# Kernel optimization log

Hardware: AMD Instinct MI355X
Metric: run time of the kernel (lower is better)

Reference implementation:

```python
import jax, jax.numpy as jnp
import numpy as np

N_NODES = 100000
N_EDGES = 1600000
N_GRAPHS = 2048
DIM_IN, DIM_H, DIM_FC, DIM_OUT = 128, 128, 256, 8


def _glorot(key, shape):
    fan_in, fan_out = shape[0], shape[1]
    lim = float(np.sqrt(6.0 / (fan_in + fan_out)))
    return jax.random.uniform(key, shape, jnp.float32, -lim, lim)


def setup_inputs() -> dict:
    key = jax.random.key(0)
    ks = jax.random.split(key, 16)
    x = jax.random.normal(ks[0], (N_NODES, DIM_IN), jnp.float32)
    edge_index = jax.random.randint(ks[1], (2, N_EDGES), 0, N_NODES, jnp.int64)
    batch = jnp.sort(jax.random.randint(ks[2], (N_NODES,), 0, N_GRAPHS, jnp.int64))
    inp = {"x": x, "edge_index": edge_index, "batch": batch}
    # GraphConv layers: W_rel [in,out], W_root [in,out], b [out]
    dims = [(DIM_IN, DIM_H), (DIM_H, DIM_H), (DIM_H, DIM_H), (DIM_H, DIM_H)]
    for i, (di, do) in enumerate(dims, start=1):
        inp[f"W{i}_rel"] = _glorot(ks[2 + 3 * i], (di, do))
        inp[f"W{i}_root"] = _glorot(ks[3 + 3 * i], (di, do))
        inp[f"b{i}"] = jnp.zeros((do,), jnp.float32)
    inp["fc_w"] = _glorot(ks[3], (DIM_H, DIM_FC))
    inp["fc_b"] = jnp.zeros((DIM_FC,), jnp.float32)
    inp["reg_w"] = _glorot(ks[4], (DIM_FC, DIM_OUT))
    inp["reg_b"] = jnp.zeros((DIM_OUT,), jnp.float32)
    return inp


def _graph_conv(x, src, dst, w_rel, w_root, b):
    # PyG GraphConv (aggr='add'): out_i = W_rel @ sum_{j->i} x_j + W_root @ x_i + b
    agg = jax.ops.segment_sum(x[src], dst, num_segments=N_NODES)  # [N, d_in]
    return agg @ w_rel + x @ w_root + b


def reference(x, edge_index, batch,
              W1_rel, W1_root, b1, W2_rel, W2_root, b2,
              W3_rel, W3_root, b3, W4_rel, W4_root, b4,
              fc_w, fc_b, reg_w, reg_b):
    src, dst = edge_index[0], edge_index[1]
    h = jax.nn.relu(_graph_conv(x, src, dst, W1_rel, W1_root, b1))
    h = jax.nn.relu(_graph_conv(h, src, dst, W2_rel, W2_root, b2))
    h = jax.nn.relu(_graph_conv(h, src, dst, W3_rel, W3_root, b3))
    h = jax.nn.relu(_graph_conv(h, src, dst, W4_rel, W4_root, b4))
    # global_mean_pool over graphs
    sums = jax.ops.segment_sum(h, batch, num_segments=N_GRAPHS)  # [G, d]
    cnt = jax.ops.segment_sum(jnp.ones((h.shape[0],), h.dtype), batch,
                              num_segments=N_GRAPHS)
    pooled = sums / jnp.maximum(cnt, 1.0)[:, None]
    # dropout is identity at inference
    hfc = pooled @ fc_w + fc_b
    return hfc @ reg_w + reg_b  # [G, dim_out]
```

## Files before the change

### kernel.cpp

```cpp
#include <hip/hip_runtime.h>

#define N_NODES 100000
#define N_EDGES 1600000
#define N_GRAPHS 2048
#define DIM 128

#define NBUK 196
#define BUKSH 9
#define NCH 256
#define EPB 6250
#define NMAT (NBUK * NCH)

typedef short short8v __attribute__((ext_vector_type(8)));
typedef float float4v __attribute__((ext_vector_type(4)));

__device__ __forceinline__ unsigned short f2bf(float f) {
  union { float f; unsigned u; } x; x.f = f;
  unsigned r = x.u + 0x7fffu + ((x.u >> 16) & 1u);
  return (unsigned short)(r >> 16);
}
__device__ __forceinline__ float bfhi2f(unsigned bits) {
  union { unsigned u; float f; } x; x.u = bits; return x.f;
}
__device__ __forceinline__ void accum8(float* p, uint4 v) {
  p[0] += bfhi2f(v.x << 16); p[1] += bfhi2f(v.x & 0xffff0000u);
  p[2] += bfhi2f(v.y << 16); p[3] += bfhi2f(v.y & 0xffff0000u);
  p[4] += bfhi2f(v.z << 16); p[5] += bfhi2f(v.z & 0xffff0000u);
  p[6] += bfhi2f(v.w << 16); p[7] += bfhi2f(v.w & 0xffff0000u);
}

__global__ __launch_bounds__(256) void k_bcount(const int* __restrict__ dst, int* __restrict__ cntmat) {
  __shared__ int cnt[NBUK];
  int b = blockIdx.x, t = threadIdx.x;
  if (t < NBUK) cnt[t] = 0;
  __syncthreads();
  int e0 = b * EPB;
  for (int j = t; j < EPB; j += 256) atomicAdd(&cnt[dst[e0 + j] >> BUKSH], 1);
  __syncthreads();
  if (t < NBUK) cntmat[t * NCH + b] = cnt[t];
}

__global__ __launch_bounds__(256) void k_scan1g(const int* __restrict__ in, int n,
                                                int* __restrict__ tmp, int* __restrict__ bsum) {
  __shared__ int sh[256];
  int b = blockIdx.x, t = threadIdx.x;
  int base = b * 1024 + t * 4;
  int v[4], s = 0;
#pragma unroll
  for (int i = 0; i < 4; i++) { v[i] = (base + i < n) ? in[base + i] : 0; s += v[i]; }
  sh[t] = s;
  __syncthreads();
  for (int off = 1; off < 256; off <<= 1) {
    int x = (t >= off) ? sh[t - off] : 0;
    __syncthreads();
    sh[t] += x;
    __syncthreads();
  }
  int run = sh[t] - s;
#pragma unroll
  for (int i = 0; i < 4; i++) { run += v[i]; if (base + i < n) tmp[base + i] = run; }
  if (t == 255) bsum[b] = sh[255];
}

__global__ void k_scan2g(int* __restrict__ bsum, int nb) {
  __shared__ int sh[128];
  int t = threadIdx.x;
  int v = (t < nb) ? bsum[t] : 0;
  sh[t] = v;
  __syncthreads();
  for (int off = 1; off < 128; off <<= 1) {
    int x = (t >= off) ? sh[t - off] : 0;
    __syncthreads();
    sh[t] += x;
    __syncthreads();
  }
  if (t < nb) bsum[t] = sh[t] - v;
}

__global__ __launch_bounds__(256) void k_exc(const int* __restrict__ tmp, const int* __restrict__ bsum,
                                             const int* __restrict__ in, int n, int* __restrict__ outExc) {
  int i = blockIdx.x * 256 + threadIdx.x;
  if (i < n) outExc[i] = tmp[i] + bsum[i >> 10] - in[i];
}

__global__ __launch_bounds__(256) void k_bscatter(const int* __restrict__ src, const int* __restrict__ dst,
                                                  const int* __restrict__ base, int2* __restrict__ epk) {
  __shared__ int cur[NBUK];
  int b = blockIdx.x, t = threadIdx.x;
  if (t < NBUK) cur[t] = base[t * NCH + b];
  __syncthreads();
  int e0 = b * EPB;
  for (int j = t; j < EPB; j += 256) {
    int s = src[e0 + j], d = dst[e0 + j];
    int pos = atomicAdd(&cur[d >> BUKSH], 1);
    epk[pos] = make_int2(s, d);
  }
}

__global__ __launch_bounds__(256) void k_bfinish(const int2* __restrict__ epk, const int* __restrict__ base,
                                                 int* __restrict__ rowptr, int* __restrict__ col) {
  __shared__ int a[512];
  __shared__ int sh[256];
  int k = blockIdx.x, t = threadIdx.x;
  int bstart = base[k * NCH];
  int bend = (k + 1 < NBUK) ? base[(k + 1) * NCH] : N_EDGES;
  a[t] = 0; a[t + 256] = 0;
  __syncthreads();
  for (int i = bstart + t; i < bend; i += 256) atomicAdd(&a[epk[i].y - (k << BUKSH)], 1);
  __syncthreads();
  int c0 = a[2 * t], c1 = a[2 * t + 1];
  int s = c0 + c1;
  sh[t] = s;
  __syncthreads();
  for (int off = 1; off < 256; off <<= 1) {
    int x = (t >= off) ? sh[t - off] : 0;
    __syncthreads();
    sh[t] += x;
    __syncthreads();
  }
  int excl = sh[t] - s;
  int st0 = bstart + excl;
  int st1 = st0 + c0;
  int g0 = (k << BUKSH) + 2 * t, g1 = g0 + 1;
  if (g0 < N_NODES) rowptr[g0] = st0;
  if (g1 < N_NODES) rowptr[g1] = st1;
  if (k == NBUK - 1 && t == 0) rowptr[N_NODES] = N_EDGES;
  __syncthreads();
  a[2 * t] = st0; a[2 * t + 1] = st1;
  __syncthreads();
  for (int i = bstart + t; i < bend; i += 256) {
    int2 e = epk[i];
    int pos = atomicAdd(&a[e.y - (k << BUKSH)], 1);
    col[pos] = e.x;
  }
}

__global__ __launch_bounds__(256) void k_gptr(const int* __restrict__ batch, int* __restrict__ gptr) {
  int i = blockIdx.x * 256 + threadIdx.x;
  if (i >= N_NODES) return;
  int b = batch[i];
  int a = (i == 0) ? -1 : batch[i - 1];
  for (int g = a + 1; g <= b; g++) gptr[g] = i;
  if (i == N_NODES - 1) {
    for (int g = b + 1; g <= N_GRAPHS; g++) gptr[g] = N_NODES;
  }
}

__global__ __launch_bounds__(256) void k_cvtx(const float* __restrict__ x, unsigned short* __restrict__ h) {
  int i = blockIdx.x * 256 + threadIdx.x;
  if (i < N_NODES * DIM / 4) {
    float4 v = ((const float4*)x)[i];
    unsigned lo = (unsigned)f2bf(v.x) | ((unsigned)f2bf(v.y) << 16);
    unsigned hi = (unsigned)f2bf(v.z) | ((unsigned)f2bf(v.w) << 16);
    ((uint2*)h)[i] = make_uint2(lo, hi);
  }
}

__global__ __launch_bounds__(256) void k_cvtw(const float* w0, const float* w1, const float* w2, const float* w3,
                                              const float* w4, const float* w5, const float* w6, const float* w7,
                                              unsigned short* __restrict__ wbF) {
  int i = blockIdx.x * 256 + threadIdx.x;
  if (i < 4 * 8 * 8 * 64 * 8) {
    int j = i & 7, l = (i >> 3) & 63, c = (i >> 9) & 7, kc = (i >> 12) & 7, layer = i >> 15;
    int m = layer * 2 + (kc >> 2);
    const float* w;
    switch (m) {
      case 0: w = w0; break; case 1: w = w1; break; case 2: w = w2; break; case 3: w = w3; break;
      case 4: w = w4; break; case 5: w = w5; break; case 6: w = w6; break; default: w = w7; break;
    }
    int kin = (kc & 3) * 32 + ((l >> 4) * 8) + j;
    int n = c * 16 + (l & 15);
    wbF[i] = f2bf(w[kin * 128 + n]);
  }
}

__global__ __launch_bounds__(256, 8) void k_fused(const int* __restrict__ rowptr,
                                                  const int* __restrict__ col,
                                                  const unsigned short* __restrict__ hIn,
                                                  const unsigned short* __restrict__ wbF,
                                                  const float* __restrict__ bias,
                                                  unsigned short* __restrict__ hOut) {
  __shared__ uint4 As[1024];
  const int t = threadIdx.x;
  const int wave = t >> 6, lane = t & 63;
  const int wrow0 = blockIdx.x * 64 + wave * 16;
  const int sub = lane >> 4, li = lane & 15;

  for (int ri = 0; ri < 16; ri += 2) {
    int nodeA = wrow0 + ri;
    int nodeB = nodeA + 1;
    float pA[8], pB[8];
#pragma unroll
    for (int j = 0; j < 8; j++) { pA[j] = 0.f; pB[j] = 0.f; }
    int aS1 = 0, bS1 = 0, eA = 0, eB = 0;
    if (nodeA < N_NODES) { eA = rowptr[nodeA]; aS1 = rowptr[nodeA + 1]; }
    if (nodeB < N_NODES) { eB = rowptr[nodeB]; bS1 = rowptr[nodeB + 1]; }

    while (eA + 8 <= aS1 && eB + 8 <= bS1) {
      int cA0 = col[eA + sub], cA1 = col[eA + 4 + sub];
      int cB0 = col[eB + sub], cB1 = col[eB + 4 + sub];
      uint4 vA0 = *(const uint4*)(hIn + (size_t)cA0 * DIM + li * 8);
      uint4 vA1 = *(const uint4*)(hIn + (size_t)cA1 * DIM + li * 8);
      uint4 vB0 = *(const uint4*)(hIn + (size_t)cB0 * DIM + li * 8);
      uint4 vB1 = *(const uint4*)(hIn + (size_t)cB1 * DIM + li * 8);
      accum8(pA, vA0);
      accum8(pA, vA1);
      accum8(pB, vB0);
      accum8(pB, vB1);
      eA += 8; eB += 8;
    }
    for (; eA + 16 <= aS1; eA += 16) {
      int c0 = col[eA + sub], c1 = col[eA + 4 + sub], c2 = col[eA + 8 + sub], c3 = col[eA + 12 + sub];
      uint4 v0 = *(const uint4*)(hIn + (size_t)c0 * DIM + li * 8);
      uint4 v1 = *(const uint4*)(hIn + (size_t)c1 * DIM + li * 8);
      uint4 v2 = *(const uint4*)(hIn + (size_t)c2 * DIM + li * 8);
      uint4 v3 = *(const uint4*)(hIn + (size_t)c3 * DIM + li * 8);
      accum8(pA, v0); accum8(pA, v1); accum8(pA, v2); accum8(pA, v3);
    }
    if (eA + 8 <= aS1) {
      int c0 = col[eA + sub], c1 = col[eA + 4 + sub];
      uint4 v0 = *(const uint4*)(hIn + (size_t)c0 * DIM + li * 8);
      uint4 v1 = *(const uint4*)(hIn + (size_t)c1 * DIM + li * 8);
      accum8(pA, v0); accum8(pA, v1);
      eA += 8;
    }
    if (eA + 4 <= aS1) {
      int c0 = col[eA + sub];
      uint4 v0 = *(const uint4*)(hIn + (size_t)c0 * DIM + li * 8);
      accum8(pA, v0);
      eA += 4;
    }
    if (eA + sub < aS1) {
      int c0 = col[eA + sub];
      uint4 v0 = *(const uint4*)(hIn + (size_t)c0 * DIM + li * 8);
      accum8(pA, v0);
    }
    for (; eB + 16 <= bS1; eB += 16) {
      int c0 = col[eB + sub], c1 = col[eB + 4 + sub], c2 = col[eB + 8 + sub], c3 = col[eB + 12 + sub];
      uint4 v0 = *(const uint4*)(hIn + (size_t)c0 * DIM + li * 8);
      uint4 v1 = *(const uint4*)(hIn + (size_t)c1 * DIM + li * 8);
      uint4 v2 = *(const uint4*)(hIn + (size_t)c2 * DIM + li * 8);
      uint4 v3 = *(const uint4*)(hIn + (size_t)c3 * DIM + li * 8);
      accum8(pB, v0); accum8(pB, v1); accum8(pB, v2); accum8(pB, v3);
    }
    if (eB + 8 <= bS1) {
      int c0 = col[eB + sub], c1 = col[eB + 4 + sub];
      uint4 v0 = *(const uint4*)(hIn + (size_t)c0 * DIM + li * 8);
      uint4 v1 = *(const uint4*)(hIn + (size_t)c1 * DIM + li * 8);
      accum8(pB, v0); accum8(pB, v1);
      eB += 8;
    }
    if (eB + 4 <= bS1) {
      int c0 = col[eB + sub];
      uint4 v0 = *(const uint4*)(hIn + (size_t)c0 * DIM + li * 8);
      accum8(pB, v0);
      eB += 4;
    }
    if (eB + sub < bS1) {
      int c0 = col[eB + sub];
      uint4 v0 = *(const uint4*)(hIn + (size_t)c0 * DIM + li * 8);
      accum8(pB, v0);
    }

#pragma unroll
    for (int j = 0; j < 8; j++) {
      pA[j] += __shfl_xor(pA[j], 16, 64);
      pA[j] += __shfl_xor(pA[j], 32, 64);
      pB[j] += __shfl_xor(pB[j], 16, 64);
      pB[j] += __shfl_xor(pB[j], 32, 64);
    }
    if (sub == 0) {
      uint4 oA, oB;
      oA.x = (unsigned)f2bf(pA[0]) | ((unsigned)f2bf(pA[1]) << 16);
      oA.y = (unsigned)f2bf(pA[2]) | ((unsigned)f2bf(pA[3]) << 16);
      oA.z = (unsigned)f2bf(pA[4]) | ((unsigned)f2bf(pA[5]) << 16);
      oA.w = (unsigned)f2bf(pA[6]) | ((unsigned)f2bf(pA[7]) << 16);
      oB.x = (unsigned)f2bf(pB[0]) | ((unsigned)f2bf(pB[1]) << 16);
      oB.y = (unsigned)f2bf(pB[2]) | ((unsigned)f2bf(pB[3]) << 16);
      oB.z = (unsigned)f2bf(pB[4]) | ((unsigned)f2bf(pB[5]) << 16);
      oB.w = (unsigned)f2bf(pB[6]) | ((unsigned)f2bf(pB[7]) << 16);
      As[(wave * 16 + li) * 16 + (ri ^ li)] = oA;
      As[(wave * 16 + li) * 16 + ((ri + 1) ^ li)] = oB;
    }
  }

  float4v acc[8];
#pragma unroll
  for (int c2 = 0; c2 < 8; c2++)
#pragma unroll
    for (int i = 0; i < 4; i++) acc[c2][i] = 0.f;

#pragma unroll
  for (int kc = 0; kc < 4; kc++) {
    int c = kc * 4 + sub;
    short8v afr = *(const short8v*)&As[(wave * 16 + c) * 16 + (li ^ c)];
#pragma unroll
    for (int c2 = 0; c2 < 8; c2++) {
      short8v bfr = *(const short8v*)(wbF + (size_t)((kc * 8 + c2) * 64 + lane) * 8);
      acc[c2] = __builtin_amdgcn_mfma_f32_16x16x32_bf16(afr, bfr, acc[c2], 0, 0, 0);
    }
  }

#pragma unroll
  for (int j = 0; j < 4; j++) {
    int idx = j * 64 + lane;
    int r = idx >> 4, c = idx & 15;
    int rsrc = wrow0 + r; if (rsrc > N_NODES - 1) rsrc = N_NODES - 1;
    uint4 v = *(const uint4*)(hIn + (size_t)rsrc * DIM + c * 8);
    As[(wave * 16 + c) * 16 + (r ^ c)] = v;
  }

#pragma unroll
  for (int kc = 0; kc < 4; kc++) {
    int c = kc * 4 + sub;
    short8v afr = *(const short8v*)&As[(wave * 16 + c) * 16 + (li ^ c)];
#pragma unroll
    for (int c2 = 0; c2 < 8; c2++) {
      short8v bfr = *(const short8v*)(wbF + (size_t)(((4 + kc) * 8 + c2) * 64 + lane) * 8);
      acc[c2] = __builtin_amdgcn_mfma_f32_16x16x32_bf16(afr, bfr, acc[c2], 0, 0, 0);
    }
  }

  int rbase = wrow0 + sub * 4;
#pragma unroll
  for (int c2 = 0; c2 < 8; c2++) {
    int colidx = c2 * 16 + li;
    float bv = bias[colidx];
#pragma unroll
    for (int i = 0; i < 4; i++) {
      int row = rbase + i;
      if (row < N_NODES) {
        float v = acc[c2][i] + bv;
        v = v > 0.f ? v : 0.f;
        hOut[row * DIM + colidx] = f2bf(v);
      }
    }
  }
}

__global__ __launch_bounds__(256) void k_pool(const unsigned short* __restrict__ h,
                                              const int* __restrict__ gptr,
                                              float* __restrict__ pooledMean) {
  int g = blockIdx.x * 4 + (threadIdx.x >> 6);
  if (g >= N_GRAPHS) return;
  int lane = threadIdx.x & 63;
  int li = lane & 15;
  int s0 = gptr[g], s1 = gptr[g + 1];
  float p[8];
#pragma unroll
  for (int j = 0; j < 8; j++) p[j] = 0.f;
  int f1 = s1 * 16;
  for (int f = s0 * 16 + lane; f < f1; f += 64) {
    uint4 v = ((const uint4*)h)[f];
    accum8(p, v);
  }
#pragma unroll
  for (int j = 0; j < 8; j++) {
    p[j] += __shfl_xor(p[j], 16, 64);
    p[j] += __shfl_xor(p[j], 32, 64);
  }
  float inv = (s1 > s0) ? 1.f / (float)(s1 - s0) : 0.f;
  if (lane < 16) {
    float4 o0 = make_float4(p[0] * inv, p[1] * inv, p[2] * inv, p[3] * inv);
    float4 o1 = make_float4(p[4] * inv, p[5] * inv, p[6] * inv, p[7] * inv);
    *(float4*)(pooledMean + g * DIM + li * 8) = o0;
    *(float4*)(pooledMean + g * DIM + li * 8 + 4) = o1;
  }
}

__global__ __launch_bounds__(256) void k_fc(const float* __restrict__ pooledMean,
                                            const float* __restrict__ fc_w, const float* __restrict__ fc_b,
                                            const float* __restrict__ reg_w, const float* __restrict__ reg_b,
                                            float* __restrict__ out) {
  __shared__ float sp[128];
  __shared__ float shfc[256];
  __shared__ float red[64];
  int g = blockIdx.x, t = threadIdx.x;
  if (t < 128) sp[t] = pooledMean[g * DIM + t];
  __syncthreads();
  float a = fc_b[t];
  for (int k = 0; k < 128; k++) a += sp[k] * fc_w[k * 256 + t];
  shfc[t] = a;
  __syncthreads();
  if (t < 64) {
    int o = t & 7, seg = t >> 3;
    float r = 0.f;
    for (int j = seg * 32; j < seg * 32 + 32; j++) r += shfc[j] * reg_w[j * 8 + o];
    red[t] = r;
  }
  __syncthreads();
  if (t < 8) {
    float r = reg_b[t];
    for (int s = 0; s < 8; s++) r += red[s * 8 + t];
    out[g * 8 + t] = r;
  }
}

extern "C" void kernel_launch(void* const* d_in, const int* in_sizes, int n_in,
                              void* d_out, int out_size, void* d_ws, size_t ws_size,
                              hipStream_t stream) {
  (void)in_sizes; (void)n_in; (void)out_size; (void)ws_size;
  const float* x = (const float*)d_in[0];
  const int* ei = (const int*)d_in[1];
  const int* src = ei;
  const int* dst = ei + N_EDGES;
  const int* batch = (const int*)d_in[2];
  const float* Wrel[4]  = {(const float*)d_in[3], (const float*)d_in[6], (const float*)d_in[9],  (const float*)d_in[12]};
  const float* Wroot[4] = {(const float*)d_in[4], (const float*)d_in[7], (const float*)d_in[10], (const float*)d_in[13]};
  const float* bias[4]  = {(const float*)d_in[5], (const float*)d_in[8], (const float*)d_in[11], (const float*)d_in[14]};
  const float* fc_w  = (const float*)d_in[15];
  const float* fc_b  = (const float*)d_in[16];
  const float* reg_w = (const float*)d_in[17];
  const float* reg_b = (const float*)d_in[18];
  float* out = (float*)d_out;

  char* ws = (char*)d_ws;
  size_t off = 0;
  auto alloc = [&](size_t b) -> char* {
    char* p = ws + off;
    off = (off + b + 255) & ~(size_t)255;
    return p;
  };
  int* rowptr = (int*)alloc((N_NODES + 1) * 4);
  int* cntmat = (int*)alloc((size_t)NMAT * 4);
  int* tmpB   = (int*)alloc((size_t)NMAT * 4);
  int* bsumB  = (int*)alloc(128 * 4);
  int* base   = (int*)alloc((size_t)NMAT * 4);
  int2* epk   = (int2*)alloc((size_t)N_EDGES * 8);
  int* colws  = (int*)alloc((size_t)N_EDGES * 4);
  int* gptr   = (int*)alloc((N_GRAPHS + 1) * 4);
  unsigned short* wbF = (unsigned short*)alloc((size_t)4 * 32768 * 2);
  unsigned short* h_a = (unsigned short*)alloc((size_t)N_NODES * DIM * 2);
  unsigned short* h_b = (unsigned short*)alloc((size_t)N_NODES * DIM * 2);
  float* pooled = (float*)alloc((size_t)N_GRAPHS * DIM * 4);

  k_bcount<<<NCH, 256, 0, stream>>>(dst, cntmat);
  k_scan1g<<<NMAT / 1024, 256, 0, stream>>>(cntmat, NMAT, tmpB, bsumB);
  k_scan2g<<<1, 128, 0, stream>>>(bsumB, NMAT / 1024);
  k_exc<<<(NMAT + 255) / 256, 256, 0, stream>>>(tmpB, bsumB, cntmat, NMAT, base);
  k_bscatter<<<NCH, 256, 0, stream>>>(src, dst, base, epk);
  k_bfinish<<<NBUK, 256, 0, stream>>>(epk, base, rowptr, colws);

  k_gptr<<<(N_NODES + 255) / 256, 256, 0, stream>>>(batch, gptr);
  k_cvtx<<<(N_NODES * DIM / 4 + 255) / 256, 256, 0, stream>>>(x, h_a);
  k_cvtw<<<(4 * 32768 + 255) / 256, 256, 0, stream>>>(
      Wrel[0], Wroot[0], Wrel[1], Wroot[1], Wrel[2], Wroot[2], Wrel[3], Wroot[3], wbF);

  unsigned short* h_in = h_a;
  unsigned short* h_out = h_b;
  const int FB = (N_NODES + 63) / 64;
  for (int l = 0; l < 4; l++) {
    k_fused<<<FB, 256, 0, stream>>>(rowptr, colws, h_in, wbF + (size_t)l * 32768, bias[l], h_out);
    unsigned short* t2 = h_in; h_in = h_out; h_out = t2;
  }

  k_pool<<<(N_GRAPHS + 3) / 4, 256, 0, stream>>>(h_in, gptr, pooled);
  k_fc<<<N_GRAPHS, 256, 0, stream>>>(pooled, fc_w, fc_b, reg_w, reg_b, out);
}
```

Before: 506.3 us.

## Build CSR with two-pass radix sort so neighbour lists come out sorted by source

The CSR build becomes a two-pass bucket sort. Edges are first bucketed by source, then stably re-bucketed by destination, so each node's neighbour list is ordered by source index. Edge records are packed into 32-bit words instead of int2, which halves the scatter traffic. The aim is better cache locality for the row gathers in the four fused layers, at the cost of extra count, scan and scatter kernels in preprocessing.

Result: slower. 535.6 us (+5.8%).

```diff
diff --git a/kernel.cpp b/kernel.cpp
--- a/kernel.cpp
+++ b/kernel.cpp
@@ -10,6 +10,7 @@
 #define NCH 256
 #define EPB 6250
 #define NMAT (NBUK * NCH)
+#define NMATD (NBUK * NBUK)
 
 typedef short short8v __attribute__((ext_vector_type(8)));
 typedef float float4v __attribute__((ext_vector_type(4)));
@@ -29,13 +30,14 @@
   p[6] += bfhi2f(v.w << 16); p[7] += bfhi2f(v.w & 0xffff0000u);
 }
 
-__global__ __launch_bounds__(256) void k_bcount(const int* __restrict__ dst, int* __restrict__ cntmat) {
+
+__global__ __launch_bounds__(256) void k_bcount(const int* __restrict__ key, int* __restrict__ cntmat) {
   __shared__ int cnt[NBUK];
   int b = blockIdx.x, t = threadIdx.x;
   if (t < NBUK) cnt[t] = 0;
   __syncthreads();
   int e0 = b * EPB;
-  for (int j = t; j < EPB; j += 256) atomicAdd(&cnt[dst[e0 + j] >> BUKSH], 1);
+  for (int j = t; j < EPB; j += 256) atomicAdd(&cnt[key[e0 + j] >> BUKSH], 1);
   __syncthreads();
   if (t < NBUK) cntmat[t * NCH + b] = cnt[t];
 }
@@ -83,30 +85,67 @@
   if (i < n) outExc[i] = tmp[i] + bsum[i >> 10] - in[i];
 }
 
-__global__ __launch_bounds__(256) void k_bscatter(const int* __restrict__ src, const int* __restrict__ dst,
-                                                  const int* __restrict__ base, int2* __restrict__ epk) {
+__global__ __launch_bounds__(256) void k_bscatterS(const int* __restrict__ src, const int* __restrict__ dst,
+                                                   const int* __restrict__ baseS, unsigned* __restrict__ epkS) {
   __shared__ int cur[NBUK];
   int b = blockIdx.x, t = threadIdx.x;
-  if (t < NBUK) cur[t] = base[t * NCH + b];
+  if (t < NBUK) cur[t] = baseS[t * NCH + b];
   __syncthreads();
   int e0 = b * EPB;
   for (int j = t; j < EPB; j += 256) {
     int s = src[e0 + j], d = dst[e0 + j];
+    int pos = atomicAdd(&cur[s >> BUKSH], 1);
+    epkS[pos] = ((unsigned)(s & 511) << 17) | (unsigned)d;
+  }
+}
+
+__global__ __launch_bounds__(256) void k_bcountD(const unsigned* __restrict__ epkS,
+                                                 const int* __restrict__ baseS,
+                                                 int* __restrict__ cntmatD) {
+  __shared__ int cnt[NBUK];
+  int b = blockIdx.x, t = threadIdx.x;
+  if (t < NBUK) cnt[t] = 0;
+  __syncthreads();
+  int bstart = baseS[b * NCH];
+  int bend = (b + 1 < NBUK) ? baseS[(b + 1) * NCH] : N_EDGES;
+  for (int i = bstart + t; i < bend; i += 256) {
+    int d = epkS[i] & 0x1FFFF;
+    atomicAdd(&cnt[d >> BUKSH], 1);
+  }
+  __syncthreads();
+  if (t < NBUK) cntmatD[t * NBUK + b] = cnt[t];
+}
+
+__global__ __launch_bounds__(256) void k_bscatterD(const unsigned* __restrict__ epkS,
+                                                   const int* __restrict__ baseS,
+                                                   const int* __restrict__ baseD,
+                                                   unsigned* __restrict__ epkD) {
+  __shared__ int cur[NBUK];
+  int b = blockIdx.x, t = threadIdx.x;
+  if (t < NBUK) cur[t] = baseD[t * NBUK + b];
+  __syncthreads();
+  int bstart = baseS[b * NCH];
+  int bend = (b + 1 < NBUK) ? baseS[(b + 1) * NCH] : N_EDGES;
+  for (int i = bstart + t; i < bend; i += 256) {
+    unsigned pk = epkS[i];
+    int d = pk & 0x1FFFF;
+    int s = (b << BUKSH) | (int)(pk >> 17);
     int pos = atomicAdd(&cur[d >> BUKSH], 1);
-    epk[pos] = make_int2(s, d);
-  }
-}
-
-__global__ __launch_bounds__(256) void k_bfinish(const int2* __restrict__ epk, const int* __restrict__ base,
-                                                 int* __restrict__ rowptr, int* __restrict__ col) {
+    epkD[pos] = ((unsigned)(d & 511) << 17) | (unsigned)s;
+  }
+}
+
+__global__ __launch_bounds__(256) void k_bfinishD(const unsigned* __restrict__ epkD,
+                                                  const int* __restrict__ baseD,
+                                                  int* __restrict__ rowptr, int* __restrict__ col) {
   __shared__ int a[512];
   __shared__ int sh[256];
   int k = blockIdx.x, t = threadIdx.x;
-  int bstart = base[k * NCH];
-  int bend = (k + 1 < NBUK) ? base[(k + 1) * NCH] : N_EDGES;
+  int bstart = baseD[k * NBUK];
+  int bend = (k + 1 < NBUK) ? baseD[(k + 1) * NBUK] : N_EDGES;
   a[t] = 0; a[t + 256] = 0;
   __syncthreads();
-  for (int i = bstart + t; i < bend; i += 256) atomicAdd(&a[epk[i].y - (k << BUKSH)], 1);
+  for (int i = bstart + t; i < bend; i += 256) atomicAdd(&a[epkD[i] >> 17], 1);
   __syncthreads();
   int c0 = a[2 * t], c1 = a[2 * t + 1];
   int s = c0 + c1;
@@ -129,9 +168,9 @@
   a[2 * t] = st0; a[2 * t + 1] = st1;
   __syncthreads();
   for (int i = bstart + t; i < bend; i += 256) {
-    int2 e = epk[i];
-    int pos = atomicAdd(&a[e.y - (k << BUKSH)], 1);
-    col[pos] = e.x;
+    unsigned pk = epkD[i];
+    int pos = atomicAdd(&a[pk >> 17], 1);
+    col[pos] = (int)(pk & 0x1FFFF);
   }
 }
 
@@ -421,25 +460,34 @@
     off = (off + b + 255) & ~(size_t)255;
     return p;
   };
-  int* rowptr = (int*)alloc((N_NODES + 1) * 4);
-  int* cntmat = (int*)alloc((size_t)NMAT * 4);
-  int* tmpB   = (int*)alloc((size_t)NMAT * 4);
-  int* bsumB  = (int*)alloc(128 * 4);
-  int* base   = (int*)alloc((size_t)NMAT * 4);
-  int2* epk   = (int2*)alloc((size_t)N_EDGES * 8);
-  int* colws  = (int*)alloc((size_t)N_EDGES * 4);
-  int* gptr   = (int*)alloc((N_GRAPHS + 1) * 4);
+  int* rowptr  = (int*)alloc((N_NODES + 1) * 4);
+  int* cntmat  = (int*)alloc((size_t)NMAT * 4);
+  int* tmpB    = (int*)alloc((size_t)NMAT * 4);
+  int* bsumB   = (int*)alloc(128 * 4);
+  int* baseS   = (int*)alloc((size_t)NMAT * 4);
+  int* cntmatD = (int*)alloc((size_t)NMATD * 4);
+  int* baseD   = (int*)alloc((size_t)NMATD * 4);
+  unsigned* epkS = (unsigned*)alloc((size_t)N_EDGES * 4);
+  unsigned* epkD = (unsigned*)alloc((size_t)N_EDGES * 4);
+  int* colws   = (int*)alloc((size_t)N_EDGES * 4);
+  int* gptr    = (int*)alloc((N_GRAPHS + 1) * 4);
   unsigned short* wbF = (unsigned short*)alloc((size_t)4 * 32768 * 2);
   unsigned short* h_a = (unsigned short*)alloc((size_t)N_NODES * DIM * 2);
   unsigned short* h_b = (unsigned short*)alloc((size_t)N_NODES * DIM * 2);
   float* pooled = (float*)alloc((size_t)N_GRAPHS * DIM * 4);
 
-  k_bcount<<<NCH, 256, 0, stream>>>(dst, cntmat);
+  k_bcount<<<NCH, 256, 0, stream>>>(src, cntmat);
   k_scan1g<<<NMAT / 1024, 256, 0, stream>>>(cntmat, NMAT, tmpB, bsumB);
   k_scan2g<<<1, 128, 0, stream>>>(bsumB, NMAT / 1024);
-  k_exc<<<(NMAT + 255) / 256, 256, 0, stream>>>(tmpB, bsumB, cntmat, NMAT, base);
-  k_bscatter<<<NCH, 256, 0, stream>>>(src, dst, base, epk);
-  k_bfinish<<<NBUK, 256, 0, stream>>>(epk, base, rowptr, colws);
+  k_exc<<<(NMAT + 255) / 256, 256, 0, stream>>>(tmpB, bsumB, cntmat, NMAT, baseS);
+  k_bscatterS<<<NCH, 256, 0, stream>>>(src, dst, baseS, epkS);
+
+  k_bcountD<<<NBUK, 256, 0, stream>>>(epkS, baseS, cntmatD);
+  k_scan1g<<<(NMATD + 1023) / 1024, 256, 0, stream>>>(cntmatD, NMATD, tmpB, bsumB);
+  k_scan2g<<<1, 128, 0, stream>>>(bsumB, (NMATD + 1023) / 1024);
+  k_exc<<<(NMATD + 255) / 256, 256, 0, stream>>>(tmpB, bsumB, cntmatD, NMATD, baseD);
+  k_bscatterD<<<NBUK, 256, 0, stream>>>(epkS, baseS, baseD, epkD);
+  k_bfinishD<<<NBUK, 256, 0, stream>>>(epkD, baseD, rowptr, colws);
 
   k_gptr<<<(N_NODES + 255) / 256, 256, 0, stream>>>(batch, gptr);
   k_cvtx<<<(N_NODES * DIM / 4 + 255) / 256, 256, 0, stream>>>(x, h_a);
```

## Replace bucketed CSR build with direct global-atomic degree count and scatter

Applied to the files above, without the earlier changes.

Replaces the two-level bucketed counting sort for building the CSR with a direct per-node degree count using global atomics, a scan over node degrees, and a scatter of source indices via per-node atomic cursors. This removes the intermediate packed edge buffer and the bucket-finish pass, cutting memory traffic and kernel count. In exchange it relies on many global atomics and yields a non-deterministic neighbor order within each row. The final FC kernel is also restructured to process 16 graphs per block, reusing each fc_w load across graphs.

New measurement: 664.9 us. 31.3% more time.

```diff
diff --git a/kernel.cpp b/kernel.cpp
--- a/kernel.cpp
+++ b/kernel.cpp
@@ -4,12 +4,6 @@
 #define N_EDGES 1600000
 #define N_GRAPHS 2048
 #define DIM 128
-
-#define NBUK 196
-#define BUKSH 9
-#define NCH 256
-#define EPB 6250
-#define NMAT (NBUK * NCH)
 
 typedef short short8v __attribute__((ext_vector_type(8)));
 typedef float float4v __attribute__((ext_vector_type(4)));
@@ -29,15 +23,15 @@
   p[6] += bfhi2f(v.w << 16); p[7] += bfhi2f(v.w & 0xffff0000u);
 }
 
-__global__ __launch_bounds__(256) void k_bcount(const int* __restrict__ dst, int* __restrict__ cntmat) {
-  __shared__ int cnt[NBUK];
-  int b = blockIdx.x, t = threadIdx.x;
-  if (t < NBUK) cnt[t] = 0;
-  __syncthreads();
-  int e0 = b * EPB;
-  for (int j = t; j < EPB; j += 256) atomicAdd(&cnt[dst[e0 + j] >> BUKSH], 1);
-  __syncthreads();
-  if (t < NBUK) cntmat[t * NCH + b] = cnt[t];
+
+__global__ __launch_bounds__(256) void k_zero(int* __restrict__ p, int n) {
+  int i = blockIdx.x * 256 + threadIdx.x;
+  if (i < n) p[i] = 0;
+}
+
+__global__ __launch_bounds__(256) void k_dcnt(const int* __restrict__ dst, int* __restrict__ deg) {
+  int e = blockIdx.x * 256 + threadIdx.x;
+  if (e < N_EDGES) atomicAdd(&deg[dst[e]], 1);
 }
 
 __global__ __launch_bounds__(256) void k_scan1g(const int* __restrict__ in, int n,
@@ -77,61 +71,24 @@
   if (t < nb) bsum[t] = sh[t] - v;
 }
 
-__global__ __launch_bounds__(256) void k_exc(const int* __restrict__ tmp, const int* __restrict__ bsum,
-                                             const int* __restrict__ in, int n, int* __restrict__ outExc) {
+__global__ __launch_bounds__(256) void k_excR(const int* __restrict__ tmp, const int* __restrict__ bsum,
+                                              const int* __restrict__ deg, int n,
+                                              int* __restrict__ rowptr, int* __restrict__ cur) {
   int i = blockIdx.x * 256 + threadIdx.x;
-  if (i < n) outExc[i] = tmp[i] + bsum[i >> 10] - in[i];
-}
-
-__global__ __launch_bounds__(256) void k_bscatter(const int* __restrict__ src, const int* __restrict__ dst,
-                                                  const int* __restrict__ base, int2* __restrict__ epk) {
-  __shared__ int cur[NBUK];
-  int b = blockIdx.x, t = threadIdx.x;
-  if (t < NBUK) cur[t] = base[t * NCH + b];
-  __syncthreads();
-  int e0 = b * EPB;
-  for (int j = t; j < EPB; j += 256) {
-    int s = src[e0 + j], d = dst[e0 + j];
-    int pos = atomicAdd(&cur[d >> BUKSH], 1);
-    epk[pos] = make_int2(s, d);
-  }
-}
-
-__global__ __launch_bounds__(256) void k_bfinish(const int2* __restrict__ epk, const int* __restrict__ base,
-                                                 int* __restrict__ rowptr, int* __restrict__ col) {
-  __shared__ int a[512];
-  __shared__ int sh[256];
-  int k = blockIdx.x, t = threadIdx.x;
-  int bstart = base[k * NCH];
-  int bend = (k + 1 < NBUK) ? base[(k + 1) * NCH] : N_EDGES;
-  a[t] = 0; a[t + 256] = 0;
-  __syncthreads();
-  for (int i = bstart + t; i < bend; i += 256) atomicAdd(&a[epk[i].y - (k << BUKSH)], 1);
-  __syncthreads();
-  int c0 = a[2 * t], c1 = a[2 * t + 1];
-  int s = c0 + c1;
-  sh[t] = s;
-  __syncthreads();
-  for (int off = 1; off < 256; off <<= 1) {
-    int x = (t >= off) ? sh[t - off] : 0;
-    __syncthreads();
-    sh[t] += x;
-    __syncthreads();
-  }
-  int excl = sh[t] - s;
-  int st0 = bstart + excl;
-  int st1 = st0 + c0;
-  int g0 = (k << BUKSH) + 2 * t, g1 = g0 + 1;
-  if (g0 < N_NODES) rowptr[g0] = st0;
-  if (g1 < N_NODES) rowptr[g1] = st1;
-  if (k == NBUK - 1 && t == 0) rowptr[N_NODES] = N_EDGES;
-  __syncthreads();
-  a[2 * t] = st0; a[2 * t + 1] = st1;
-  __syncthreads();
-  for (int i = bstart + t; i < bend; i += 256) {
-    int2 e = epk[i];
-    int pos = atomicAdd(&a[e.y - (k << BUKSH)], 1);
-    col[pos] = e.x;
+  if (i < n) {
+    int ex = tmp[i] + bsum[i >> 10] - deg[i];
+    rowptr[i] = ex;
+    cur[i] = ex;
+    if (i == n - 1) rowptr[n] = ex + deg[i];
+  }
+}
+
+__global__ __launch_bounds__(256) void k_escatter(const int* __restrict__ src, const int* __restrict__ dst,
+                                                  int* __restrict__ cur, int* __restrict__ col) {
+  int e = blockIdx.x * 256 + threadIdx.x;
+  if (e < N_EDGES) {
+    int pos = atomicAdd(&cur[dst[e]], 1);
+    col[pos] = src[e];
   }
 }
 
@@ -368,31 +325,33 @@
   }
 }
 
-__global__ __launch_bounds__(256) void k_fc(const float* __restrict__ pooledMean,
-                                            const float* __restrict__ fc_w, const float* __restrict__ fc_b,
-                                            const float* __restrict__ reg_w, const float* __restrict__ reg_b,
-                                            float* __restrict__ out) {
-  __shared__ float sp[128];
-  __shared__ float shfc[256];
-  __shared__ float red[64];
-  int g = blockIdx.x, t = threadIdx.x;
-  if (t < 128) sp[t] = pooledMean[g * DIM + t];
+#define GPB 16
+__global__ __launch_bounds__(256) void k_fc2(const float* __restrict__ pooledMean,
+                                             const float* __restrict__ fc_w, const float* __restrict__ fc_b,
+                                             const float* __restrict__ reg_w, const float* __restrict__ reg_b,
+                                             float* __restrict__ out) {
+  __shared__ float sp[GPB][128];
+  __shared__ float shfc[GPB][257];
+  int g0 = blockIdx.x * GPB, t = threadIdx.x;
+  for (int k = t; k < GPB * 128; k += 256) sp[k >> 7][k & 127] = pooledMean[g0 * 128 + k];
   __syncthreads();
-  float a = fc_b[t];
-  for (int k = 0; k < 128; k++) a += sp[k] * fc_w[k * 256 + t];
-  shfc[t] = a;
+  float a[GPB];
+  float fb = fc_b[t];
+#pragma unroll
+  for (int g = 0; g < GPB; g++) a[g] = fb;
+  for (int k = 0; k < 128; k++) {
+    float w = fc_w[k * 256 + t];
+#pragma unroll
+    for (int g = 0; g < GPB; g++) a[g] += sp[g][k] * w;
+  }
+#pragma unroll
+  for (int g = 0; g < GPB; g++) shfc[g][t] = a[g];
   __syncthreads();
-  if (t < 64) {
-    int o = t & 7, seg = t >> 3;
-    float r = 0.f;
-    for (int j = seg * 32; j < seg * 32 + 32; j++) r += shfc[j] * reg_w[j * 8 + o];
-    red[t] = r;
-  }
-  __syncthreads();
-  if (t < 8) {
-    float r = reg_b[t];
-    for (int s = 0; s < 8; s++) r += red[s * 8 + t];
-    out[g * 8 + t] = r;
+  if (t < GPB * 8) {
+    int g = t >> 3, o = t & 7;
+    float r = reg_b[o];
+    for (int j = 0; j < 256; j++) r += shfc[g][j] * reg_w[j * 8 + o];
+    out[(g0 + g) * 8 + o] = r;
   }
 }
 
@@ -422,11 +381,10 @@
     return p;
   };
   int* rowptr = (int*)alloc((N_NODES + 1) * 4);
-  int* cntmat = (int*)alloc((size_t)NMAT * 4);
-  int* tmpB   = (int*)alloc((size_t)NMAT * 4);
+  int* deg    = (int*)alloc((size_t)N_NODES * 4);
+  int* cur    = (int*)alloc((size_t)N_NODES * 4);
+  int* tmpB   = (int*)alloc((size_t)N_NODES * 4);
   int* bsumB  = (int*)alloc(128 * 4);
-  int* base   = (int*)alloc((size_t)NMAT * 4);
-  int2* epk   = (int2*)alloc((size_t)N_EDGES * 8);
   int* colws  = (int*)alloc((size_t)N_EDGES * 4);
   int* gptr   = (int*)alloc((N_GRAPHS + 1) * 4);
   unsigned short* wbF = (unsigned short*)alloc((size_t)4 * 32768 * 2);
@@ -434,12 +392,13 @@
   unsigned short* h_b = (unsigned short*)alloc((size_t)N_NODES * DIM * 2);
   float* pooled = (float*)alloc((size_t)N_GRAPHS * DIM * 4);
 
-  k_bcount<<<NCH, 256, 0, stream>>>(dst, cntmat);
-  k_scan1g<<<NMAT / 1024, 256, 0, stream>>>(cntmat, NMAT, tmpB, bsumB);
-  k_scan2g<<<1, 128, 0, stream>>>(bsumB, NMAT / 1024);
-  k_exc<<<(NMAT + 255) / 256, 256, 0, stream>>>(tmpB, bsumB, cntmat, NMAT, base);
-  k_bscatter<<<NCH, 256, 0, stream>>>(src, dst, base, epk);
-  k_bfinish<<<NBUK, 256, 0, stream>>>(epk, base, rowptr, colws);
+  const int NSCAN = (N_NODES + 1023) / 1024;
+  k_zero<<<(N_NODES + 255) / 256, 256, 0, stream>>>(deg, N_NODES);
+  k_dcnt<<<(N_EDGES + 255) / 256, 256, 0, stream>>>(dst, deg);
+  k_scan1g<<<NSCAN, 256, 0, stream>>>(deg, N_NODES, tmpB, bsumB);
+  k_scan2g<<<1, 128, 0, stream>>>(bsumB, NSCAN);
+  k_excR<<<(N_NODES + 255) / 256, 256, 0, stream>>>(tmpB, bsumB, deg, N_NODES, rowptr, cur);
+  k_escatter<<<(N_EDGES + 255) / 256, 256, 0, stream>>>(src, dst, cur, colws);
 
   k_gptr<<<(N_NODES + 255) / 256, 256, 0, stream>>>(batch, gptr);
   k_cvtx<<<(N_NODES * DIM / 4 + 255) / 256, 256, 0, stream>>>(x, h_a);
@@ -455,5 +414,5 @@
   }
 
   k_pool<<<(N_GRAPHS + 3) / 4, 256, 0, stream>>>(h_in, gptr, pooled);
-  k_fc<<<N_GRAPHS, 256, 0, stream>>>(pooled, fc_w, fc_b, reg_w, reg_b, out);
-}
+  k_fc2<<<N_GRAPHS / GPB, 256, 0, stream>>>(pooled, fc_w, fc_b, reg_w, reg_b, out);
+}
```
